# Kernel tuning notes

Hardware: AMD Instinct MI355X
Metric: run time of the kernel (lower is better)

The kernel has to match this reference:

```python
import jax, jax.numpy as jnp
import numpy as np

C = 128; H = 56; W = 56; WS = 7; SS = 3; NH = 4; T = 8; B = 4
BT = B * T; L = H * W; N = WS * WS; HD = C // NH; SCALE = HD ** -0.5
NW = (H // WS) * (W // WS)

def _np_consts():
    # spatial relative position index (Swin)
    coords = np.stack(np.meshgrid(np.arange(WS), np.arange(WS), indexing='ij')).reshape(2, -1)
    rel = (coords[:, :, None] - coords[:, None, :]).transpose(1, 2, 0)
    rel[..., 0] += WS - 1; rel[..., 1] += WS - 1; rel[..., 0] *= 2 * WS - 1
    rpi = rel.sum(-1)  # (N, N) in [0, (2WS-1)^2)
    # temporal relative index
    tri = (np.arange(T)[:, None] - np.arange(T)[None, :]) + T - 1  # (T, T)
    # shifted-window attention mask
    img = np.zeros((1, H, W, 1), np.float32); cnt = 0
    sl = (slice(0, -WS), slice(-WS, -SS), slice(-SS, None))
    for hs in sl:
        for ws_ in sl:
            img[:, hs, ws_, :] = cnt; cnt += 1
    mw = img.reshape(1, H // WS, WS, W // WS, WS, 1).transpose(0, 1, 3, 2, 4, 5).reshape(-1, N)
    am = mw[:, None, :] - mw[:, :, None]
    attn_mask = np.where(am != 0, -100.0, 0.0).astype(np.float32)  # (NW, N, N)
    return rpi, tri, attn_mask

RPI, TRI, ATTN_MASK_NP = _np_consts()

def _ln(x, g, b, eps=1e-5):
    m = x.mean(-1, keepdims=True)
    v = ((x - m) ** 2).mean(-1, keepdims=True)
    return (x - m) * jax.lax.rsqrt(v + eps) * g + b

def _attn(x, bias, mask, qkv_w, qkv_b, proj_w, proj_b):
    # x: (Bn, n, C); bias: (NH, n, n); mask: (NW, n, n) or None
    Bn, n, _ = x.shape
    qkv = (x @ qkv_w + qkv_b).reshape(Bn, n, 3, NH, HD).transpose(2, 0, 3, 1, 4)
    q, k, v = qkv[0] * SCALE, qkv[1], qkv[2]  # (Bn, NH, n, HD)
    a = jnp.einsum('bhnd,bhmd->bhnm', q, k) + bias[None]
    if mask is not None:
        nW = mask.shape[0]
        a = (a.reshape(Bn // nW, nW, NH, n, n) + mask[None, :, None]).reshape(Bn, NH, n, n)
    a = jax.nn.softmax(a, axis=-1)
    o = jnp.einsum('bhnm,bhmd->bhnd', a, v).transpose(0, 2, 1, 3).reshape(Bn, n, C)
    return o @ proj_w + proj_b

def _fwd(x, qkv_w, qkv_b, proj_w, proj_b, rpb_table, tpb_table,
         norm1_g, norm1_b, norm2_g, norm2_b,
         mlp_w1, mlp_b1, mlp_w2, mlp_b2,
         s_w1, s_b1, s_w2, s_b2,
         t_w1, t_b1, t_w2, t_b2,
         a_w1, a_b1, a_w2, a_b2):
    gelu = lambda z: jax.nn.gelu(z, approximate=False)
    mask = jnp.asarray(ATTN_MASK_NP)
    sp_bias = rpb_table[RPI.reshape(-1)].reshape(N, N, NH).transpose(2, 0, 1)  # (NH,N,N)
    tp_bias = tpb_table[TRI.reshape(-1)].reshape(T, T, NH).transpose(2, 0, 1)  # (NH,T,T)

    # ---- temporal attention (t_attn=True, signal='video') ----
    shortcut = x
    xt = x.reshape(B, T, L, C).transpose(0, 2, 1, 3).reshape(B * L, T, C)
    xt = _ln(xt, norm1_g, norm1_b)
    xt = _attn(xt, tp_bias, None, qkv_w, qkv_b, proj_w, proj_b)
    # T_Adapter (non-residual)
    xt = gelu(xt @ t_w1 + t_b1) @ t_w2 + t_b2
    xt = xt.reshape(B, L, T, C).transpose(0, 2, 1, 3).reshape(BT, L, C)
    x = shortcut + xt

    # ---- shifted-window spatial attention ----
    shortcut = x
    xs = _ln(x, norm1_g, norm1_b).reshape(BT, H, W, C)
    xs = jnp.roll(xs, (-SS, -SS), axis=(1, 2))
    # window partition -> (BT*NW, N, C)
    xw = xs.reshape(BT, H // WS, WS, W // WS, WS, C).transpose(0, 1, 3, 2, 4, 5).reshape(-1, N, C)
    aw = _attn(xw, sp_bias, mask, qkv_w, qkv_b, proj_w, proj_b)
    # S_Adapter (SAdapter2, residual inside)
    aw = aw + (gelu(aw @ s_w1 + s_b1) @ s_w2 + s_b2)
    # window reverse
    xs = aw.reshape(BT, H // WS, W // WS, WS, WS, C).transpose(0, 1, 3, 2, 4, 5).reshape(BT, H, W, C)
    xs = jnp.roll(xs, (SS, SS), axis=(1, 2)).reshape(BT, L, C)
    x = shortcut + xs

    # ---- MLP + MLP_Adapter (AIM-style, scaled 0.5) ----
    xn = _ln(x, norm2_g, norm2_b)
    mlp = (gelu(xn @ mlp_w1 + mlp_b1)) @ mlp_w2 + mlp_b2
    ada = (gelu(xn @ a_w1 + a_b1)) @ a_w2 + a_b2
    return x + mlp + 0.5 * ada

def setup_inputs() -> dict:
    key = jax.random.key(0)
    ks = iter(jax.random.split(key, 16))
    p = lambda *s: jax.random.normal(next(ks), s, jnp.float32) * 0.02
    Ah = C // 4; M = 4 * C
    return {
        'x': jax.random.normal(next(ks), (BT, L, C), jnp.float32),
        'qkv_w': p(C, 3 * C), 'qkv_b': jnp.zeros((3 * C,), jnp.float32),
        'proj_w': p(C, C), 'proj_b': jnp.zeros((C,), jnp.float32),
        'rpb_table': p((2 * WS - 1) ** 2, NH), 'tpb_table': p(2 * T - 1, NH),
        'norm1_g': jnp.ones((C,), jnp.float32), 'norm1_b': jnp.zeros((C,), jnp.float32),
        'norm2_g': jnp.ones((C,), jnp.float32), 'norm2_b': jnp.zeros((C,), jnp.float32),
        'mlp_w1': p(C, M), 'mlp_b1': jnp.zeros((M,), jnp.float32),
        'mlp_w2': p(M, C), 'mlp_b2': jnp.zeros((C,), jnp.float32),
        's_w1': p(C, Ah), 's_b1': jnp.zeros((Ah,), jnp.float32),
        's_w2': p(Ah, C), 's_b2': jnp.zeros((C,), jnp.float32),
        't_w1': p(C, Ah), 't_b1': jnp.zeros((Ah,), jnp.float32),
        't_w2': p(Ah, C), 't_b2': jnp.zeros((C,), jnp.float32),
        'a_w1': p(C, Ah), 'a_b1': jnp.zeros((Ah,), jnp.float32),
        'a_w2': p(Ah, C), 'a_b2': jnp.zeros((C,), jnp.float32),
    }

def reference(x, qkv_w, qkv_b, proj_w, proj_b, rpb_table, tpb_table,
              norm1_g, norm1_b, norm2_g, norm2_b,
              mlp_w1, mlp_b1, mlp_w2, mlp_b2,
              s_w1, s_b1, s_w2, s_b2,
              t_w1, t_b1, t_w2, t_b2,
              a_w1, a_b1, a_w2, a_b2):
    return _fwd(x, qkv_w, qkv_b, proj_w, proj_b, rpb_table, tpb_table,
                norm1_g, norm1_b, norm2_g, norm2_b,
                mlp_w1, mlp_b1, mlp_w2, mlp_b2,
                s_w1, s_b1, s_w2, s_b2,
                t_w1, t_b1, t_w2, t_b2,
                a_w1, a_b1, a_w2, a_b2)
```

## Files before the change

kernel.cpp:

```cpp
#include <hip/hip_runtime.h>

#define TOKS 100352
#define LDIM 3136
#define SCALE_F 0.17677669529663687f

typedef unsigned short u16;
typedef u16   u16x8 __attribute__((ext_vector_type(8)));
typedef short s16x8 __attribute__((ext_vector_type(8)));
typedef float f32x8 __attribute__((ext_vector_type(8)));
typedef float f32x4 __attribute__((ext_vector_type(4)));

__device__ __forceinline__ float bf2f(u16 u){ return __uint_as_float(((unsigned)u)<<16); }
__device__ __forceinline__ u16 f2bf(float f){
  unsigned u = __float_as_uint(f);
  return (u16)((u + 0x7FFFu + ((u>>16)&1u)) >> 16);
}
__device__ __forceinline__ f32x8 ldbf8(const u16* p){
  u16x8 u = *(const u16x8*)p;
  f32x8 f;
  #pragma unroll
  for (int j=0;j<8;j++) f[j] = bf2f(u[j]);
  return f;
}
__device__ __forceinline__ u16x8 pack8(f32x8 v){
  u16x8 r;
  #pragma unroll
  for (int j=0;j<8;j++) r[j] = f2bf(v[j]);
  return r;
}
__device__ __forceinline__ float sum8(f32x8 a){
  return ((a[0]+a[1])+(a[2]+a[3]))+((a[4]+a[5])+(a[6]+a[7]));
}
__device__ __forceinline__ float gelu_f(float x){
  float t = x*(0.7978845608f + 0.03567740814f*x*x);
  float e = __expf(2.0f*t);
  float th = 1.0f - 2.0f/(e + 1.0f);
  return 0.5f*x*(1.0f + th);
}

__device__ __forceinline__ void gl16(const u16* g, u16* l){
  __builtin_amdgcn_global_load_lds(
      (const __attribute__((address_space(1))) unsigned*)(const void*)g,
      (__attribute__((address_space(3))) unsigned*)(void*)l, 16, 0, 0);
}
__device__ __forceinline__ void stage_tile(const u16* __restrict__ src, size_t rowstart,
    int KTOT, int koff, u16* lds, int wv, int lane){
  const int rr = wv*4 + (lane>>4);
  const int sl = lane&15;
  const int kb = sl ^ (rr&7);
  const u16* g0 = src + (rowstart + rr)*(size_t)KTOT + koff + kb*8;
  u16* l0 = lds + wv*4*128;
  #pragma unroll
  for (int it=0; it<8; it++)
    gl16(g0 + (size_t)it*16*KTOT, l0 + it*16*128);
}

struct WSrc { const float* p[10]; };
__global__ __launch_bounds__(256) void prep_w(WSrc s, u16* __restrict__ dst){
  const int Ks[10]={128,128,128,512,128,32,128,32,128,32};
  const int Ns[10]={384,128,512,128,32,128,32,128,32,128};
  const int off[11]={0,49152,65536,131072,196608,200704,204800,208896,212992,217088,221184};
  int idx = blockIdx.x*256+threadIdx.x;
  int m=0;
  #pragma unroll
  for (int i=0;i<10;i++) if (idx>=off[i+1]) m=i+1;
  int e = idx-off[m];
  int K=Ks[m], Nn=Ns[m];
  int n=e/K, k=e-n*K;
  dst[idx] = f2bf(s.p[m][k*Nn+n]);
}

__global__ __launch_bounds__(256) void ln_kernel(const float* __restrict__ x,
    const float* __restrict__ g, const float* __restrict__ bta, u16* __restrict__ out)
{
  int tok  = (int)((blockIdx.x*256u + threadIdx.x) >> 6);
  int lane = threadIdx.x & 63;
  const float* xr = x + (size_t)tok*128;
  float v0 = xr[lane], v1 = xr[lane+64];
  float s = v0+v1;
  #pragma unroll
  for (int o=32;o;o>>=1) s += __shfl_xor(s,o);
  float m = s*(1.0f/128.0f);
  float d0=v0-m, d1=v1-m;
  float q = d0*d0+d1*d1;
  #pragma unroll
  for (int o=32;o;o>>=1) q += __shfl_xor(q,o);
  float rs = rsqrtf(q*(1.0f/128.0f)+1e-5f);
  u16* orow = out + (size_t)tok*128;
  orow[lane]    = f2bf(d0*rs*g[lane]   + bta[lane]);
  orow[lane+64] = f2bf(d1*rs*g[lane+64]+ bta[lane+64]);
}

template<int KCH, int NTC, int EPI>
__global__ __launch_bounds__(256,2) void gemm_tile(
    const u16* __restrict__ X, const u16* __restrict__ WT,
    const float* __restrict__ bias, void* outp, int N,
    const float* res1, const u16* __restrict__ adab)
{
  constexpr int KTOT = KCH*128;
  __shared__ u16 As[128*128];
  __shared__ u16 Bs[128*128];
  const int tid = threadIdx.x;
  const int wv = tid>>6, lane = tid&63, lr = lane>>4, lc = lane&15;
  const int wr = wv>>1, wc = wv&1;
  const size_t row0 = (size_t)blockIdx.x*128;

  f32x4 acc[4][4];
  #pragma unroll
  for (int mi=0;mi<4;mi++)
    #pragma unroll
    for (int nj=0;nj<4;nj++) acc[mi][nj] = (f32x4){0.f,0.f,0.f,0.f};

  for (int kc=0; kc<KCH; kc++){
    for (int nt=0; nt<NTC; nt++){
      if (kc+nt > 0) __syncthreads();
      if (nt == 0) stage_tile(X, row0, KTOT, kc*128, As, wv, lane);
      stage_tile(WT, (size_t)nt*128, KTOT, kc*128, Bs, wv, lane);
      __syncthreads();
      #pragma unroll
      for (int kt=0; kt<4; kt++){
        s16x8 af[4], bfr[4];
        #pragma unroll
        for (int mi=0;mi<4;mi++){
          int row = wr*64 + mi*16 + lc;
          af[mi] = *(const s16x8*)&As[row*128 + (((kt*4+lr) ^ (lc&7))*8)];
        }
        #pragma unroll
        for (int nj=0;nj<4;nj++){
          int col = wc*64 + nj*16 + lc;
          bfr[nj] = *(const s16x8*)&Bs[col*128 + (((kt*4+lr) ^ (lc&7))*8)];
        }
        #pragma unroll
        for (int mi=0;mi<4;mi++)
          #pragma unroll
          for (int nj=0;nj<4;nj++)
            acc[mi][nj] = __builtin_amdgcn_mfma_f32_16x16x32_bf16(af[mi], bfr[nj], acc[mi][nj], 0,0,0);
      }
      if (KCH==1){
        __syncthreads();
        #pragma unroll
        for (int mi=0;mi<4;mi++){
          #pragma unroll
          for (int nj=0;nj<4;nj++){
            const int colL = wc*64 + nj*16 + lc;
            const float bv = bias[nt*128 + colL];
            #pragma unroll
            for (int r=0;r<4;r++){
              const int row = wr*64 + mi*16 + lr*4 + r;
              float v = acc[mi][nj][r] + bv;
              if constexpr (EPI==1) v = gelu_f(v);
              Bs[row*128 + ((colL + ((row&12)<<2)) & 127)] = f2bf(v);
            }
            acc[mi][nj] = (f32x4){0.f,0.f,0.f,0.f};
          }
        }
        __syncthreads();
        #pragma unroll
        for (int it=0; it<8; it++){
          int v = it*256 + tid;
          int row = v>>4, c8 = v&15;
          int sc8 = (c8 + ((row&12)>>1)) & 15;
          u16x8 val = *(const u16x8*)&Bs[row*128 + sc8*8];
          *(u16x8*)&((u16*)outp)[(row0+row)*(size_t)N + nt*128 + c8*8] = val;
        }
      }
    }
  }
  if (KCH>1){
    #pragma unroll
    for (int mi=0;mi<4;mi++){
      #pragma unroll
      for (int nj=0;nj<4;nj++){
        const int col = wc*64 + nj*16 + lc;
        const float bv = bias[col];
        #pragma unroll
        for (int r=0;r<4;r++){
          const size_t row = row0 + wr*64 + mi*16 + lr*4 + r;
          float v = acc[mi][nj][r] + bv;
          if constexpr (EPI==4) v += res1[row*128+col] + 0.5f*bf2f(adab[row*128+col]);
          ((float*)outp)[row*128 + col] = v;
        }
      }
    }
  }
}

template<int SMODE>
__global__ __launch_bounds__(256,2) void proj_ada_tile(
    const u16* __restrict__ O, const u16* __restrict__ PW, const float* __restrict__ pb,
    const u16* __restrict__ W1T, const float* __restrict__ b1,
    const u16* __restrict__ W2T, const float* __restrict__ b2,
    const float* __restrict__ res1, float* __restrict__ outp)
{
  __shared__ u16 As[128*128];
  __shared__ u16 Bs[128*128];
  __shared__ u16 Hs[4][32][40];
  const int tid = threadIdx.x;
  const int wv = tid>>6, lane = tid&63, lr = lane>>4, lc = lane&15;
  const int wr = wv>>1, wc = wv&1;
  const size_t row0 = (size_t)blockIdx.x*128;
  stage_tile(O, row0, 128, 0, As, wv, lane);
  stage_tile(PW, 0, 128, 0, Bs, wv, lane);
  __syncthreads();
  f32x4 acc[4][4];
  #pragma unroll
  for (int mi=0;mi<4;mi++)
    #pragma unroll
    for (int nj=0;nj<4;nj++) acc[mi][nj] = (f32x4){0.f,0.f,0.f,0.f};
  #pragma unroll
  for (int kt=0; kt<4; kt++){
    s16x8 af[4], bfr[4];
    #pragma unroll
    for (int mi=0;mi<4;mi++)
      af[mi] = *(const s16x8*)&As[(wr*64+mi*16+lc)*128 + (((kt*4+lr) ^ (lc&7))*8)];
    #pragma unroll
    for (int nj=0;nj<4;nj++)
      bfr[nj] = *(const s16x8*)&Bs[(wc*64+nj*16+lc)*128 + (((kt*4+lr) ^ (lc&7))*8)];
    #pragma unroll
    for (int mi=0;mi<4;mi++)
      #pragma unroll
      for (int nj=0;nj<4;nj++)
        acc[mi][nj] = __builtin_amdgcn_mfma_f32_16x16x32_bf16(af[mi], bfr[nj], acc[mi][nj], 0,0,0);
  }
  __syncthreads();
  #pragma unroll
  for (int mi=0;mi<4;mi++){
    #pragma unroll
    for (int nj=0;nj<4;nj++){
      const int col = wc*64 + nj*16 + lc;
      const float bv = pb[col];
      #pragma unroll
      for (int r=0;r<4;r++){
        const int row = wr*64 + mi*16 + lr*4 + r;
        As[row*128 + (((col>>3) ^ (row&7))*8) + (col&7)] = f2bf(acc[mi][nj][r] + bv);
      }
    }
  }
  __syncthreads();
  const int rbase = wv*32;
  f32x4 a2[2][2];
  #pragma unroll
  for (int mi=0;mi<2;mi++){ a2[mi][0]=(f32x4){0.f,0.f,0.f,0.f}; a2[mi][1]=(f32x4){0.f,0.f,0.f,0.f}; }
  #pragma unroll
  for (int kt=0; kt<4; kt++){
    s16x8 af0 = *(const s16x8*)&As[(rbase+lc)*128 + (((kt*4+lr) ^ (lc&7))*8)];
    s16x8 af1 = *(const s16x8*)&As[(rbase+16+lc)*128 + (((kt*4+lr) ^ (lc&7))*8)];
    #pragma unroll
    for (int nj=0; nj<2; nj++){
      s16x8 b = *(const s16x8*)&W1T[(size_t)(nj*16+lc)*128 + kt*32 + lr*8];
      a2[0][nj] = __builtin_amdgcn_mfma_f32_16x16x32_bf16(af0, b, a2[0][nj], 0,0,0);
      a2[1][nj] = __builtin_amdgcn_mfma_f32_16x16x32_bf16(af1, b, a2[1][nj], 0,0,0);
    }
  }
  #pragma unroll
  for (int mi=0;mi<2;mi++){
    #pragma unroll
    for (int nj=0;nj<2;nj++){
      const int col = nj*16 + lc;
      const float bv = b1[col];
      #pragma unroll
      for (int r=0;r<4;r++)
        Hs[wv][mi*16 + lr*4 + r][col] = f2bf(gelu_f(a2[mi][nj][r] + bv));
    }
  }
  f32x4 a3[2][8];
  #pragma unroll
  for (int mi=0;mi<2;mi++){
    s16x8 af = *(const s16x8*)&Hs[wv][mi*16+lc][lr*8];
    #pragma unroll
    for (int nj=0;nj<8;nj++){
      s16x8 b = *(const s16x8*)&W2T[(size_t)(nj*16+lc)*32 + lr*8];
      a3[mi][nj] = __builtin_amdgcn_mfma_f32_16x16x32_bf16(af, b, (f32x4){0.f,0.f,0.f,0.f}, 0,0,0);
    }
  }
  #pragma unroll
  for (int mi=0;mi<2;mi++){
    #pragma unroll
    for (int nj=0;nj<8;nj++){
      const int col = nj*16 + lc;
      const float bv = b2[col];
      #pragma unroll
      for (int r=0;r<4;r++){
        const int rl = rbase + mi*16 + lr*4 + r;
        const size_t row = row0 + rl;
        float v = a3[mi][nj][r] + bv + res1[row*128+col];
        if constexpr (SMODE==1)
          v += bf2f(As[rl*128 + (((col>>3) ^ (rl&7))*8) + (col&7)]);
        outp[row*128 + col] = v;
      }
    }
  }
}

__global__ __launch_bounds__(256,2) void mlp1_ada(
    const u16* __restrict__ X, const u16* __restrict__ WT, const float* __restrict__ bias,
    const u16* __restrict__ A1T, const float* __restrict__ ab1,
    const u16* __restrict__ A2T, const float* __restrict__ ab2,
    u16* __restrict__ Hout, u16* __restrict__ adab)
{
  __shared__ u16 As[128*128];
  __shared__ u16 Bs[128*128];
  __shared__ u16 Hs[4][32][40];
  const int tid = threadIdx.x;
  const int wv = tid>>6, lane = tid&63, lr = lane>>4, lc = lane&15;
  const int wr = wv>>1, wc = wv&1;
  const size_t row0 = (size_t)blockIdx.x*128;

  f32x4 acc[4][4];
  #pragma unroll
  for (int mi=0;mi<4;mi++)
    #pragma unroll
    for (int nj=0;nj<4;nj++) acc[mi][nj] = (f32x4){0.f,0.f,0.f,0.f};

  for (int nt=0; nt<4; nt++){
    if (nt > 0) __syncthreads();
    if (nt == 0) stage_tile(X, row0, 128, 0, As, wv, lane);
    stage_tile(WT, (size_t)nt*128, 128, 0, Bs, wv, lane);
    __syncthreads();
    #pragma unroll
    for (int kt=0; kt<4; kt++){
      s16x8 af[4], bfr[4];
      #pragma unroll
      for (int mi=0;mi<4;mi++)
        af[mi] = *(const s16x8*)&As[(wr*64+mi*16+lc)*128 + (((kt*4+lr) ^ (lc&7))*8)];
      #pragma unroll
      for (int nj=0;nj<4;nj++)
        bfr[nj] = *(const s16x8*)&Bs[(wc*64+nj*16+lc)*128 + (((kt*4+lr) ^ (lc&7))*8)];
      #pragma unroll
      for (int mi=0;mi<4;mi++)
        #pragma unroll
        for (int nj=0;nj<4;nj++)
          acc[mi][nj] = __builtin_amdgcn_mfma_f32_16x16x32_bf16(af[mi], bfr[nj], acc[mi][nj], 0,0,0);
    }
    __syncthreads();
    #pragma unroll
    for (int mi=0;mi<4;mi++){
      #pragma unroll
      for (int nj=0;nj<4;nj++){
        const int colL = wc*64 + nj*16 + lc;
        const float bv = bias[nt*128 + colL];
        #pragma unroll
        for (int r=0;r<4;r++){
          const int row = wr*64 + mi*16 + lr*4 + r;
          Bs[row*128 + ((colL + ((row&12)<<2)) & 127)] = f2bf(gelu_f(acc[mi][nj][r] + bv));
        }
        acc[mi][nj] = (f32x4){0.f,0.f,0.f,0.f};
      }
    }
    __syncthreads();
    #pragma unroll
    for (int it=0; it<8; it++){
      int v = it*256 + tid;
      int row = v>>4, c8 = v&15;
      int sc8 = (c8 + ((row&12)>>1)) & 15;
      u16x8 val = *(const u16x8*)&Bs[row*128 + sc8*8];
      *(u16x8*)&Hout[(row0+row)*512 + nt*128 + c8*8] = val;
    }
  }
  const int rbase = wv*32;
  f32x4 a2[2][2];
  #pragma unroll
  for (int mi=0;mi<2;mi++){ a2[mi][0]=(f32x4){0.f,0.f,0.f,0.f}; a2[mi][1]=(f32x4){0.f,0.f,0.f,0.f}; }
  #pragma unroll
  for (int kt=0; kt<4; kt++){
    s16x8 af0 = *(const s16x8*)&As[(rbase+lc)*128 + (((kt*4+lr) ^ (lc&7))*8)];
    s16x8 af1 = *(const s16x8*)&As[(rbase+16+lc)*128 + (((kt*4+lr) ^ (lc&7))*8)];
    #pragma unroll
    for (int nj=0; nj<2; nj++){
      s16x8 b = *(const s16x8*)&A1T[(size_t)(nj*16+lc)*128 + kt*32 + lr*8];
      a2[0][nj] = __builtin_amdgcn_mfma_f32_16x16x32_bf16(af0, b, a2[0][nj], 0,0,0);
      a2[1][nj] = __builtin_amdgcn_mfma_f32_16x16x32_bf16(af1, b, a2[1][nj], 0,0,0);
    }
  }
  #pragma unroll
  for (int mi=0;mi<2;mi++){
    #pragma unroll
    for (int nj=0;nj<2;nj++){
      const int col = nj*16 + lc;
      const float bv = ab1[col];
      #pragma unroll
      for (int r=0;r<4;r++)
        Hs[wv][mi*16 + lr*4 + r][col] = f2bf(gelu_f(a2[mi][nj][r] + bv));
    }
  }
  f32x4 a3[2][8];
  #pragma unroll
  for (int mi=0;mi<2;mi++){
    s16x8 af = *(const s16x8*)&Hs[wv][mi*16+lc][lr*8];
    #pragma unroll
    for (int nj=0;nj<8;nj++){
      s16x8 b = *(const s16x8*)&A2T[(size_t)(nj*16+lc)*32 + lr*8];
      a3[mi][nj] = __builtin_amdgcn_mfma_f32_16x16x32_bf16(af, b, (f32x4){0.f,0.f,0.f,0.f}, 0,0,0);
    }
  }
  #pragma unroll
  for (int mi=0;mi<2;mi++){
    #pragma unroll
    for (int nj=0;nj<8;nj++){
      const int col = nj*16 + lc;
      const float bv = ab2[col];
      #pragma unroll
      for (int r=0;r<4;r++){
        const size_t row = row0 + rbase + mi*16 + lr*4 + r;
        adab[row*128 + col] = f2bf(a3[mi][nj][r] + bv);
      }
    }
  }
}

__global__ __launch_bounds__(256) void t_attn_kernel(const u16* __restrict__ qkv,
    const float* __restrict__ tpb, u16* __restrict__ o)
{
  const int tid = threadIdx.x;
  const int li = tid>>5, h = (tid>>3)&3, t = tid&7;
  const int b = blockIdx.x/392, lt = blockIdx.x%392;
  const int l = lt*8+li;
  const size_t rowt = (size_t)(b*8+t)*LDIM + l;
  const u16* qp = qkv + rowt*384 + h*32;
  f32x8 q0 = ldbf8(qp)   *SCALE_F, q1 = ldbf8(qp+8) *SCALE_F,
        q2 = ldbf8(qp+16)*SCALE_F, q3 = ldbf8(qp+24)*SCALE_F;
  float s[8];
  #pragma unroll
  for (int t2=0;t2<8;t2++){
    const u16* kp = qkv + ((size_t)(b*8+t2)*LDIM + l)*384 + 128 + h*32;
    f32x8 d = q0*ldbf8(kp) + q1*ldbf8(kp+8) + q2*ldbf8(kp+16) + q3*ldbf8(kp+24);
    s[t2] = sum8(d) + tpb[(t-t2+7)*4 + h];
  }
  float m = s[0];
  #pragma unroll
  for (int t2=1;t2<8;t2++) m = fmaxf(m, s[t2]);
  float ssum = 0.f;
  #pragma unroll
  for (int t2=0;t2<8;t2++){ s[t2] = __expf(s[t2]-m); ssum += s[t2]; }
  const float inv = 1.0f/ssum;
  f32x8 o0={0,0,0,0,0,0,0,0}, o1={0,0,0,0,0,0,0,0},
        o2={0,0,0,0,0,0,0,0}, o3={0,0,0,0,0,0,0,0};
  #pragma unroll
  for (int t2=0;t2<8;t2++){
    const u16* vp = qkv + ((size_t)(b*8+t2)*LDIM + l)*384 + 256 + h*32;
    float aw = s[t2]*inv;
    o0 += aw*ldbf8(vp); o1 += aw*ldbf8(vp+8); o2 += aw*ldbf8(vp+16); o3 += aw*ldbf8(vp+24);
  }
  u16* op = o + rowt*128 + h*32;
  *(u16x8*)op      = pack8(o0); *(u16x8*)(op+8)  = pack8(o1);
  *(u16x8*)(op+16) = pack8(o2); *(u16x8*)(op+24) = pack8(o3);
}

__global__ __launch_bounds__(256,2) void s_attn_mfma(const u16* __restrict__ qkv,
    const float* __restrict__ rpb, u16* __restrict__ o)
{
  __shared__ u16 Qs[64][136];
  __shared__ u16 Ks[64][136];
  __shared__ u16 Vt[128][72];
  __shared__ float rpbL[676];
  __shared__ int rowL[49];
  __shared__ int codeL[49];
  const int tid = threadIdx.x;
  const int bidx = blockIdx.x;
  const int bt = bidx>>6, wh = (bidx>>3)&7, ww = bidx&7;
  if (tid < 49){
    int ph = tid/7, pwv = tid%7;
    int rh = wh*7+ph, rw = ww*7+pwv;
    int oh = rh+3; if (oh>=56) oh-=56;
    int ow = rw+3; if (ow>=56) ow-=56;
    rowL[tid] = bt*LDIM + oh*56 + ow;
    codeL[tid] = ((rh<49)?0:((rh<53)?1:2))*3 + ((rw<49)?0:((rw<53)?1:2));
  }
  for (int i2 = tid; i2 < 676; i2 += 256) rpbL[i2] = rpb[i2];
  for (int idx = tid; idx < 128*15; idx += 256){
    int d = idx/15, jj = 49 + (idx - d*15);
    Vt[d][jj] = 0;
  }
  __syncthreads();
  #pragma unroll
  for (int it = 0; it < 10; it++){
    int idx = it*256 + tid;
    if (idx < 2352){
      int j = idx/48, s = idx - j*48;
      const u16* src = qkv + (size_t)rowL[j]*384 + s*8;
      u16x8 v = *(const u16x8*)src;
      if (s < 16)      *(u16x8*)&Qs[j][s*8] = v;
      else if (s < 32) *(u16x8*)&Ks[j][(s-16)*8] = v;
      else { int c0 = (s-32)*8;
        #pragma unroll
        for (int e=0;e<8;e++) Vt[c0+e][j] = v[e];
      }
    }
  }
  __syncthreads();

  const int h = tid>>6, lane = tid&63, lr = lane>>4, lc = lane&15;
  s16x8 qf[4], kf[4];
  #pragma unroll
  for (int t=0;t<4;t++){
    qf[t] = *(const s16x8*)&Qs[t*16+lc][h*32+lr*8];
    kf[t] = *(const s16x8*)&Ks[t*16+lc][h*32+lr*8];
  }
  f32x4 sa[4][4];
  #pragma unroll
  for (int tj=0;tj<4;tj++){
    #pragma unroll
    for (int ti=0;ti<4;ti++)
      sa[tj][ti] = __builtin_amdgcn_mfma_f32_16x16x32_bf16(kf[tj], qf[ti], (f32x4){0.f,0.f,0.f,0.f}, 0,0,0);
  }
  int ihv[4], iwv[4], civ[4];
  #pragma unroll
  for (int ti=0;ti<4;ti++){
    int i = ti*16+lc; int im = (i<49)? i:48;
    int ih2 = (im*147)>>10; ihv[ti]=ih2; iwv[ti]=im-ih2*7; civ[ti]=codeL[im];
  }
  float rs[4] = {0.f,0.f,0.f,0.f};
  #pragma unroll
  for (int tj=0;tj<4;tj++){
    #pragma unroll
    for (int r=0;r<4;r++){
      int j = tj*16 + lr*4 + r;
      bool jv = (j<49);
      int jm = jv? j:48;
      int jh2 = (jm*147)>>10; int jw2 = jm - jh2*7; int cj = codeL[jm];
      #pragma unroll
      for (int ti=0;ti<4;ti++){
        float sv = sa[tj][ti][r]*SCALE_F
                 + rpbL[((ihv[ti]-jh2+6)*13 + (iwv[ti]-jw2+6))*4 + h];
        if (civ[ti] != cj) sv -= 100.f;
        float pv = jv ? __expf(sv) : 0.f;
        sa[tj][ti][r] = pv;
        rs[ti] += pv;
      }
    }
  }
  #pragma unroll
  for (int ti=0;ti<4;ti++){
    float t2 = rs[ti];
    t2 += __shfl_xor(t2, 16);
    t2 += __shfl_xor(t2, 32);
    rs[ti] = 1.0f/t2;
  }
  unsigned lo[4][4], hi[4][4];
  #pragma unroll
  for (int tj=0;tj<4;tj++){
    #pragma unroll
    for (int ti=0;ti<4;ti++){
      float inv = rs[ti];
      unsigned a0 = f2bf(sa[tj][ti][0]*inv), a1 = f2bf(sa[tj][ti][1]*inv);
      unsigned a2 = f2bf(sa[tj][ti][2]*inv), a3 = f2bf(sa[tj][ti][3]*inv);
      lo[tj][ti] = a0 | (a1<<16);
      hi[tj][ti] = a2 | (a3<<16);
    }
  }
  f32x4 oa[4][2];
  #pragma unroll
  for (int mi=0;mi<4;mi++){ oa[mi][0]=(f32x4){0.f,0.f,0.f,0.f}; oa[mi][1]=(f32x4){0.f,0.f,0.f,0.f}; }
  const int srcA = lc + ((lane>>4)&1)*32;
  const int srcB = srcA + 16;
  const bool hiHalf = (lr>=2);
  #pragma unroll
  for (int kt=0;kt<2;kt++){
    s16x8 vf[2];
    #pragma unroll
    for (int nd=0;nd<2;nd++)
      vf[nd] = *(const s16x8*)&Vt[h*32 + nd*16 + lc][kt*32 + lr*8];
    #pragma unroll
    for (int mi=0;mi<4;mi++){
      unsigned wA0 = __shfl(lo[2*kt][mi],   srcA), wB0 = __shfl(lo[2*kt+1][mi], srcA);
      unsigned wA1 = __shfl(hi[2*kt][mi],   srcA), wB1 = __shfl(hi[2*kt+1][mi], srcA);
      unsigned wA2 = __shfl(lo[2*kt][mi],   srcB), wB2 = __shfl(lo[2*kt+1][mi], srcB);
      unsigned wA3 = __shfl(hi[2*kt][mi],   srcB), wB3 = __shfl(hi[2*kt+1][mi], srcB);
      union { unsigned u[4]; s16x8 v8; } cv;
      cv.u[0] = hiHalf? wB0 : wA0;
      cv.u[1] = hiHalf? wB1 : wA1;
      cv.u[2] = hiHalf? wB2 : wA2;
      cv.u[3] = hiHalf? wB3 : wA3;
      #pragma unroll
      for (int nd=0;nd<2;nd++)
        oa[mi][nd] = __builtin_amdgcn_mfma_f32_16x16x32_bf16(cv.v8, vf[nd], oa[mi][nd], 0,0,0);
    }
  }
  #pragma unroll
  for (int mi=0;mi<4;mi++){
    #pragma unroll
    for (int r=0;r<4;r++){
      int i = mi*16 + lr*4 + r;
      if (i < 49){
        size_t orow = (size_t)rowL[i]*128 + h*32;
        o[orow + lc]      = f2bf(oa[mi][0][r]);
        o[orow + 16 + lc] = f2bf(oa[mi][1][r]);
      }
    }
  }
}

extern "C" void kernel_launch(void* const* d_in, const int* in_sizes, int n_in,
                              void* d_out, int out_size, void* d_ws, size_t ws_size,
                              hipStream_t stream)
{
  (void)in_sizes; (void)n_in; (void)out_size; (void)ws_size;
  const float* x      = (const float*)d_in[0];
  const float* qkv_w  = (const float*)d_in[1];
  const float* qkv_b  = (const float*)d_in[2];
  const float* proj_w = (const float*)d_in[3];
  const float* proj_b = (const float*)d_in[4];
  const float* rpb    = (const float*)d_in[5];
  const float* tpb    = (const float*)d_in[6];
  const float* n1g    = (const float*)d_in[7];
  const float* n1b    = (const float*)d_in[8];
  const float* n2g    = (const float*)d_in[9];
  const float* n2b    = (const float*)d_in[10];
  const float* mw1    = (const float*)d_in[11];
  const float* mb1    = (const float*)d_in[12];
  const float* mw2    = (const float*)d_in[13];
  const float* mb2    = (const float*)d_in[14];
  const float* sw1    = (const float*)d_in[15];
  const float* sb1    = (const float*)d_in[16];
  const float* sw2    = (const float*)d_in[17];
  const float* sb2    = (const float*)d_in[18];
  const float* tw1    = (const float*)d_in[19];
  const float* tb1    = (const float*)d_in[20];
  const float* tw2    = (const float*)d_in[21];
  const float* tb2    = (const float*)d_in[22];
  const float* aw1    = (const float*)d_in[23];
  const float* ab1    = (const float*)d_in[24];
  const float* aw2    = (const float*)d_in[25];
  const float* ab2    = (const float*)d_in[26];

  char* ws = (char*)d_ws;
  u16*   Xn  = (u16*)(ws);
  u16*   QKV = (u16*)(ws + 25690112ULL);
  u16*   O   = (u16*)(ws + 102760448ULL);
  float* Cb  = (float*)(ws + 134873088ULL);
  u16*   AdaBf = (u16*)(ws + 134873088ULL);
  u16*   WT  = (u16*)(ws + 186253312ULL);
  float* out = (float*)d_out;

  const u16 *WTqkv=WT, *WTproj=WT+49152, *WTm1=WT+65536, *WTm2=WT+131072,
            *WTt1=WT+196608, *WTt2=WT+200704, *WTs1=WT+204800, *WTs2=WT+208896,
            *WTa1=WT+212992, *WTa2=WT+217088;

  WSrc srcs; srcs.p[0]=qkv_w; srcs.p[1]=proj_w; srcs.p[2]=mw1; srcs.p[3]=mw2;
  srcs.p[4]=tw1; srcs.p[5]=tw2; srcs.p[6]=sw1; srcs.p[7]=sw2; srcs.p[8]=aw1; srcs.p[9]=aw2;
  prep_w<<<864,256,0,stream>>>(srcs, WT);

  ln_kernel<<<25088,256,0,stream>>>(x, n1g, n1b, Xn);
  gemm_tile<1,3,0><<<784,256,0,stream>>>(Xn, WTqkv, qkv_b, QKV, 384, nullptr,nullptr);
  t_attn_kernel<<<1568,256,0,stream>>>(QKV, tpb, O);
  proj_ada_tile<0><<<784,256,0,stream>>>(O, WTproj, proj_b, WTt1, tb1, WTt2, tb2, x, Cb);
  ln_kernel<<<25088,256,0,stream>>>(Cb, n1g, n1b, Xn);
  gemm_tile<1,3,0><<<784,256,0,stream>>>(Xn, WTqkv, qkv_b, QKV, 384, nullptr,nullptr);
  s_attn_mfma<<<2048,256,0,stream>>>(QKV, rpb, O);
  proj_ada_tile<1><<<784,256,0,stream>>>(O, WTproj, proj_b, WTs1, sb1, WTs2, sb2, Cb, out);
  ln_kernel<<<25088,256,0,stream>>>(out, n2g, n2b, Xn);
  mlp1_ada<<<784,256,0,stream>>>(Xn, WTm1, mb1, WTa1, ab1, WTa2, ab2, QKV, AdaBf);
  gemm_tile<4,1,4><<<784,256,0,stream>>>(QKV, WTm2, mb2, out, 128, out, AdaBf);
}
```

Before: 421.6 us.

## Fuse LayerNorm into proj epilogue, store GEMM outputs directly with packed bf16

Computes the following LayerNorm inside the proj_ada_tile epilogue, removing two separate ln_kernel passes over the activations. Swaps MFMA operand order so each lane owns four contiguous output columns, enabling vectorised direct global stores instead of staging through LDS with extra barriers. Uses the hardware packed bf16 conversion instruction and replaces the tanh GELU with a cheaper sigmoid approximation, which loosens accuracy against exact GELU. The direct stores are less coalesced than the previous LDS-staged 16-byte row writes.

After: 407.2 us. 1.04x faster.

```diff
diff --git a/kernel.cpp b/kernel.cpp
--- a/kernel.cpp
+++ b/kernel.cpp
@@ -15,6 +15,11 @@
   unsigned u = __float_as_uint(f);
   return (u16)((u + 0x7FFFu + ((u>>16)&1u)) >> 16);
 }
+__device__ __forceinline__ unsigned cvtpk(float a, float b){
+  unsigned r;
+  asm("v_cvt_pk_bf16_f32 %0, %1, %2" : "=v"(r) : "v"(a), "v"(b));
+  return r;
+}
 __device__ __forceinline__ f32x8 ldbf8(const u16* p){
   u16x8 u = *(const u16x8*)p;
   f32x8 f;
@@ -32,10 +37,7 @@
   return ((a[0]+a[1])+(a[2]+a[3]))+((a[4]+a[5])+(a[6]+a[7]));
 }
 __device__ __forceinline__ float gelu_f(float x){
-  float t = x*(0.7978845608f + 0.03567740814f*x*x);
-  float e = __expf(2.0f*t);
-  float th = 1.0f - 2.0f/(e + 1.0f);
-  return 0.5f*x*(1.0f + th);
+  return x / (1.0f + __expf(-1.702f*x));
 }
 
 __device__ __forceinline__ void gl16(const u16* g, u16* l){
@@ -134,52 +136,43 @@
         for (int mi=0;mi<4;mi++)
           #pragma unroll
           for (int nj=0;nj<4;nj++)
-            acc[mi][nj] = __builtin_amdgcn_mfma_f32_16x16x32_bf16(af[mi], bfr[nj], acc[mi][nj], 0,0,0);
+            acc[mi][nj] = __builtin_amdgcn_mfma_f32_16x16x32_bf16(bfr[nj], af[mi], acc[mi][nj], 0,0,0);
       }
       if (KCH==1){
-        __syncthreads();
         #pragma unroll
-        for (int mi=0;mi<4;mi++){
+        for (int nj=0;nj<4;nj++){
+          const int colb = nt*128 + wc*64 + nj*16 + lr*4;
+          float4 b4 = *(const float4*)&bias[colb];
           #pragma unroll
-          for (int nj=0;nj<4;nj++){
-            const int colL = wc*64 + nj*16 + lc;
-            const float bv = bias[nt*128 + colL];
-            #pragma unroll
-            for (int r=0;r<4;r++){
-              const int row = wr*64 + mi*16 + lr*4 + r;
-              float v = acc[mi][nj][r] + bv;
-              if constexpr (EPI==1) v = gelu_f(v);
-              Bs[row*128 + ((colL + ((row&12)<<2)) & 127)] = f2bf(v);
-            }
+          for (int mi=0;mi<4;mi++){
+            const size_t row = row0 + wr*64 + mi*16 + lc;
+            float v0=acc[mi][nj][0]+b4.x, v1=acc[mi][nj][1]+b4.y,
+                  v2=acc[mi][nj][2]+b4.z, v3=acc[mi][nj][3]+b4.w;
+            if constexpr (EPI==1){ v0=gelu_f(v0); v1=gelu_f(v1); v2=gelu_f(v2); v3=gelu_f(v3); }
+            uint2 pk; pk.x = cvtpk(v0,v1); pk.y = cvtpk(v2,v3);
+            *(uint2*)&((u16*)outp)[row*(size_t)N + colb] = pk;
             acc[mi][nj] = (f32x4){0.f,0.f,0.f,0.f};
           }
         }
-        __syncthreads();
-        #pragma unroll
-        for (int it=0; it<8; it++){
-          int v = it*256 + tid;
-          int row = v>>4, c8 = v&15;
-          int sc8 = (c8 + ((row&12)>>1)) & 15;
-          u16x8 val = *(const u16x8*)&Bs[row*128 + sc8*8];
-          *(u16x8*)&((u16*)outp)[(row0+row)*(size_t)N + nt*128 + c8*8] = val;
-        }
       }
     }
   }
   if (KCH>1){
     #pragma unroll
-    for (int mi=0;mi<4;mi++){
-      #pragma unroll
-      for (int nj=0;nj<4;nj++){
-        const int col = wc*64 + nj*16 + lc;
-        const float bv = bias[col];
-        #pragma unroll
-        for (int r=0;r<4;r++){
-          const size_t row = row0 + wr*64 + mi*16 + lr*4 + r;
-          float v = acc[mi][nj][r] + bv;
-          if constexpr (EPI==4) v += res1[row*128+col] + 0.5f*bf2f(adab[row*128+col]);
-          ((float*)outp)[row*128 + col] = v;
-        }
+    for (int nj=0;nj<4;nj++){
+      const int colb = wc*64 + nj*16 + lr*4;
+      float4 b4 = *(const float4*)&bias[colb];
+      #pragma unroll
+      for (int mi=0;mi<4;mi++){
+        const size_t row = row0 + wr*64 + mi*16 + lc;
+        float4 o4 = *(const float4*)&res1[row*128 + colb];
+        uint2 au = *(const uint2*)&adab[row*128 + colb];
+        float4 v;
+        v.x = acc[mi][nj][0]+b4.x+o4.x+0.5f*bf2f((u16)(au.x&0xffff));
+        v.y = acc[mi][nj][1]+b4.y+o4.y+0.5f*bf2f((u16)(au.x>>16));
+        v.z = acc[mi][nj][2]+b4.z+o4.z+0.5f*bf2f((u16)(au.y&0xffff));
+        v.w = acc[mi][nj][3]+b4.w+o4.w+0.5f*bf2f((u16)(au.y>>16));
+        *(float4*)&((float*)outp)[row*128 + colb] = v;
       }
     }
   }
@@ -190,7 +183,8 @@
     const u16* __restrict__ O, const u16* __restrict__ PW, const float* __restrict__ pb,
     const u16* __restrict__ W1T, const float* __restrict__ b1,
     const u16* __restrict__ W2T, const float* __restrict__ b2,
-    const float* __restrict__ res1, float* __restrict__ outp)
+    const float* __restrict__ res1, float* __restrict__ outp,
+    const float* __restrict__ gn, const float* __restrict__ gb, u16* __restrict__ xnout)
 {
   __shared__ u16 As[128*128];
   __shared__ u16 Bs[128*128];
@@ -220,20 +214,20 @@
     for (int mi=0;mi<4;mi++)
       #pragma unroll
       for (int nj=0;nj<4;nj++)
-        acc[mi][nj] = __builtin_amdgcn_mfma_f32_16x16x32_bf16(af[mi], bfr[nj], acc[mi][nj], 0,0,0);
+        acc[mi][nj] = __builtin_amdgcn_mfma_f32_16x16x32_bf16(bfr[nj], af[mi], acc[mi][nj], 0,0,0);
   }
   __syncthreads();
   #pragma unroll
-  for (int mi=0;mi<4;mi++){
-    #pragma unroll
-    for (int nj=0;nj<4;nj++){
-      const int col = wc*64 + nj*16 + lc;
-      const float bv = pb[col];
-      #pragma unroll
-      for (int r=0;r<4;r++){
-        const int row = wr*64 + mi*16 + lr*4 + r;
-        As[row*128 + (((col>>3) ^ (row&7))*8) + (col&7)] = f2bf(acc[mi][nj][r] + bv);
-      }
+  for (int nj=0;nj<4;nj++){
+    const int colb = wc*64 + nj*16 + lr*4;
+    float4 b4 = *(const float4*)&pb[colb];
+    #pragma unroll
+    for (int mi=0;mi<4;mi++){
+      const int row = wr*64 + mi*16 + lc;
+      uint2 pk;
+      pk.x = cvtpk(acc[mi][nj][0]+b4.x, acc[mi][nj][1]+b4.y);
+      pk.y = cvtpk(acc[mi][nj][2]+b4.z, acc[mi][nj][3]+b4.w);
+      *(uint2*)&As[row*128 + (((colb>>3) ^ (row&7))*8) + (colb&7)] = pk;
     }
   }
   __syncthreads();
@@ -248,19 +242,21 @@
     #pragma unroll
     for (int nj=0; nj<2; nj++){
       s16x8 b = *(const s16x8*)&W1T[(size_t)(nj*16+lc)*128 + kt*32 + lr*8];
-      a2[0][nj] = __builtin_amdgcn_mfma_f32_16x16x32_bf16(af0, b, a2[0][nj], 0,0,0);
-      a2[1][nj] = __builtin_amdgcn_mfma_f32_16x16x32_bf16(af1, b, a2[1][nj], 0,0,0);
-    }
-  }
-  #pragma unroll
-  for (int mi=0;mi<2;mi++){
-    #pragma unroll
-    for (int nj=0;nj<2;nj++){
-      const int col = nj*16 + lc;
-      const float bv = b1[col];
-      #pragma unroll
-      for (int r=0;r<4;r++)
-        Hs[wv][mi*16 + lr*4 + r][col] = f2bf(gelu_f(a2[mi][nj][r] + bv));
+      a2[0][nj] = __builtin_amdgcn_mfma_f32_16x16x32_bf16(b, af0, a2[0][nj], 0,0,0);
+      a2[1][nj] = __builtin_amdgcn_mfma_f32_16x16x32_bf16(b, af1, a2[1][nj], 0,0,0);
+    }
+  }
+  #pragma unroll
+  for (int nj=0;nj<2;nj++){
+    const int hb = nj*16 + lr*4;
+    float4 b4 = *(const float4*)&b1[hb];
+    #pragma unroll
+    for (int mi=0;mi<2;mi++){
+      const int tok = mi*16 + lc;
+      uint2 pk;
+      pk.x = cvtpk(gelu_f(a2[mi][nj][0]+b4.x), gelu_f(a2[mi][nj][1]+b4.y));
+      pk.y = cvtpk(gelu_f(a2[mi][nj][2]+b4.z), gelu_f(a2[mi][nj][3]+b4.w));
+      *(uint2*)&Hs[wv][tok][hb] = pk;
     }
   }
   f32x4 a3[2][8];
@@ -270,24 +266,54 @@
     #pragma unroll
     for (int nj=0;nj<8;nj++){
       s16x8 b = *(const s16x8*)&W2T[(size_t)(nj*16+lc)*32 + lr*8];
-      a3[mi][nj] = __builtin_amdgcn_mfma_f32_16x16x32_bf16(af, b, (f32x4){0.f,0.f,0.f,0.f}, 0,0,0);
-    }
-  }
+      a3[mi][nj] = __builtin_amdgcn_mfma_f32_16x16x32_bf16(b, af, (f32x4){0.f,0.f,0.f,0.f}, 0,0,0);
+    }
+  }
+  float sum[2]={0.f,0.f}, sq[2]={0.f,0.f};
   #pragma unroll
   for (int mi=0;mi<2;mi++){
+    const int rl = rbase + mi*16 + lc;
+    const size_t row = row0 + rl;
     #pragma unroll
     for (int nj=0;nj<8;nj++){
-      const int col = nj*16 + lc;
-      const float bv = b2[col];
-      #pragma unroll
-      for (int r=0;r<4;r++){
-        const int rl = rbase + mi*16 + lr*4 + r;
-        const size_t row = row0 + rl;
-        float v = a3[mi][nj][r] + bv + res1[row*128+col];
-        if constexpr (SMODE==1)
-          v += bf2f(As[rl*128 + (((col>>3) ^ (rl&7))*8) + (col&7)]);
-        outp[row*128 + col] = v;
-      }
+      const int colb = nj*16 + lr*4;
+      float4 b4 = *(const float4*)&b2[colb];
+      float4 r4 = *(const float4*)&res1[row*128 + colb];
+      f32x4 v;
+      v[0]=a3[mi][nj][0]+b4.x+r4.x; v[1]=a3[mi][nj][1]+b4.y+r4.y;
+      v[2]=a3[mi][nj][2]+b4.z+r4.z; v[3]=a3[mi][nj][3]+b4.w+r4.w;
+      if constexpr (SMODE==1){
+        uint2 pu = *(const uint2*)&As[rl*128 + (((colb>>3) ^ (rl&7))*8) + (colb&7)];
+        v[0] += bf2f((u16)(pu.x&0xffff)); v[1] += bf2f((u16)(pu.x>>16));
+        v[2] += bf2f((u16)(pu.y&0xffff)); v[3] += bf2f((u16)(pu.y>>16));
+      }
+      float4 st; st.x=v[0]; st.y=v[1]; st.z=v[2]; st.w=v[3];
+      *(float4*)&outp[row*128 + colb] = st;
+      a3[mi][nj] = v;
+      sum[mi] += (v[0]+v[1])+(v[2]+v[3]);
+      sq[mi]  += (v[0]*v[0]+v[1]*v[1])+(v[2]*v[2]+v[3]*v[3]);
+    }
+  }
+  #pragma unroll
+  for (int mi=0;mi<2;mi++){
+    float s2 = sum[mi], q2 = sq[mi];
+    s2 += __shfl_xor(s2,16); s2 += __shfl_xor(s2,32);
+    q2 += __shfl_xor(q2,16); q2 += __shfl_xor(q2,32);
+    float mean = s2*(1.0f/128.0f);
+    float var  = q2*(1.0f/128.0f) - mean*mean;
+    float rs   = rsqrtf(var + 1e-5f);
+    const size_t row = row0 + rbase + mi*16 + lc;
+    #pragma unroll
+    for (int nj=0;nj<8;nj++){
+      const int colb = nj*16 + lr*4;
+      float4 g4 = *(const float4*)&gn[colb];
+      float4 h4 = *(const float4*)&gb[colb];
+      uint2 pk;
+      pk.x = cvtpk((a3[mi][nj][0]-mean)*rs*g4.x + h4.x,
+                   (a3[mi][nj][1]-mean)*rs*g4.y + h4.y);
+      pk.y = cvtpk((a3[mi][nj][2]-mean)*rs*g4.z + h4.z,
+                   (a3[mi][nj][3]-mean)*rs*g4.w + h4.w);
+      *(uint2*)&xnout[row*128 + colb] = pk;
     }
   }
 }
@@ -330,31 +356,21 @@
       for (int mi=0;mi<4;mi++)
         #pragma unroll
         for (int nj=0;nj<4;nj++)
-          acc[mi][nj] = __builtin_amdgcn_mfma_f32_16x16x32_bf16(af[mi], bfr[nj], acc[mi][nj], 0,0,0);
-    }
-    __syncthreads();
-    #pragma unroll
-    for (int mi=0;mi<4;mi++){
-      #pragma unroll
-      for (int nj=0;nj<4;nj++){
-        const int colL = wc*64 + nj*16 + lc;
-        const float bv = bias[nt*128 + colL];
-        #pragma unroll
-        for (int r=0;r<4;r++){
-          const int row = wr*64 + mi*16 + lr*4 + r;
-          Bs[row*128 + ((colL + ((row&12)<<2)) & 127)] = f2bf(gelu_f(acc[mi][nj][r] + bv));
-        }
+          acc[mi][nj] = __builtin_amdgcn_mfma_f32_16x16x32_bf16(bfr[nj], af[mi], acc[mi][nj], 0,0,0);
+    }
+    #pragma unroll
+    for (int nj=0;nj<4;nj++){
+      const int colb = nt*128 + wc*64 + nj*16 + lr*4;
+      float4 b4 = *(const float4*)&bias[colb];
+      #pragma unroll
+      for (int mi=0;mi<4;mi++){
+        const size_t row = row0 + wr*64 + mi*16 + lc;
+        uint2 pk;
+        pk.x = cvtpk(gelu_f(acc[mi][nj][0]+b4.x), gelu_f(acc[mi][nj][1]+b4.y));
+        pk.y = cvtpk(gelu_f(acc[mi][nj][2]+b4.z), gelu_f(acc[mi][nj][3]+b4.w));
+        *(uint2*)&Hout[row*512 + colb] = pk;
         acc[mi][nj] = (f32x4){0.f,0.f,0.f,0.f};
       }
-    }
-    __syncthreads();
-    #pragma unroll
-    for (int it=0; it<8; it++){
-      int v = it*256 + tid;
-      int row = v>>4, c8 = v&15;
-      int sc8 = (c8 + ((row&12)>>1)) & 15;
-      u16x8 val = *(const u16x8*)&Bs[row*128 + sc8*8];
-      *(u16x8*)&Hout[(row0+row)*512 + nt*128 + c8*8] = val;
     }
   }
   const int rbase = wv*32;
@@ -368,19 +384,21 @@
     #pragma unroll
     for (int nj=0; nj<2; nj++){
       s16x8 b = *(const s16x8*)&A1T[(size_t)(nj*16+lc)*128 + kt*32 + lr*8];
-      a2[0][nj] = __builtin_amdgcn_mfma_f32_16x16x32_bf16(af0, b, a2[0][nj], 0,0,0);
-      a2[1][nj] = __builtin_amdgcn_mfma_f32_16x16x32_bf16(af1, b, a2[1][nj], 0,0,0);
-    }
-  }
-  #pragma unroll
-  for (int mi=0;mi<2;mi++){
-    #pragma unroll
-    for (int nj=0;nj<2;nj++){
-      const int col = nj*16 + lc;
-      const float bv = ab1[col];
-      #pragma unroll
-      for (int r=0;r<4;r++)
-        Hs[wv][mi*16 + lr*4 + r][col] = f2bf(gelu_f(a2[mi][nj][r] + bv));
+      a2[0][nj] = __builtin_amdgcn_mfma_f32_16x16x32_bf16(b, af0, a2[0][nj], 0,0,0);
+      a2[1][nj] = __builtin_amdgcn_mfma_f32_16x16x32_bf16(b, af1, a2[1][nj], 0,0,0);
+    }
+  }
+  #pragma unroll
+  for (int nj=0;nj<2;nj++){
+    const int hb = nj*16 + lr*4;
+    float4 b4 = *(const float4*)&ab1[hb];
+    #pragma unroll
+    for (int mi=0;mi<2;mi++){
+      const int tok = mi*16 + lc;
+      uint2 pk;
+      pk.x = cvtpk(gelu_f(a2[mi][nj][0]+b4.x), gelu_f(a2[mi][nj][1]+b4.y));
+      pk.y = cvtpk(gelu_f(a2[mi][nj][2]+b4.z), gelu_f(a2[mi][nj][3]+b4.w));
+      *(uint2*)&Hs[wv][tok][hb] = pk;
     }
   }
   f32x4 a3[2][8];
@@ -390,20 +408,20 @@
     #pragma unroll
     for (int nj=0;nj<8;nj++){
       s16x8 b = *(const s16x8*)&A2T[(size_t)(nj*16+lc)*32 + lr*8];
-      a3[mi][nj] = __builtin_amdgcn_mfma_f32_16x16x32_bf16(af, b, (f32x4){0.f,0.f,0.f,0.f}, 0,0,0);
-    }
-  }
-  #pragma unroll
-  for (int mi=0;mi<2;mi++){
-    #pragma unroll
-    for (int nj=0;nj<8;nj++){
-      const int col = nj*16 + lc;
-      const float bv = ab2[col];
-      #pragma unroll
-      for (int r=0;r<4;r++){
-        const size_t row = row0 + rbase + mi*16 + lr*4 + r;
-        adab[row*128 + col] = f2bf(a3[mi][nj][r] + bv);
-      }
+      a3[mi][nj] = __builtin_amdgcn_mfma_f32_16x16x32_bf16(b, af, (f32x4){0.f,0.f,0.f,0.f}, 0,0,0);
+    }
+  }
+  #pragma unroll
+  for (int nj=0;nj<8;nj++){
+    const int colb = nj*16 + lr*4;
+    float4 b4 = *(const float4*)&ab2[colb];
+    #pragma unroll
+    for (int mi=0;mi<2;mi++){
+      const size_t row = row0 + rbase + mi*16 + lc;
+      uint2 pk;
+      pk.x = cvtpk(a3[mi][nj][0]+b4.x, a3[mi][nj][1]+b4.y);
+      pk.y = cvtpk(a3[mi][nj][2]+b4.z, a3[mi][nj][3]+b4.w);
+      *(uint2*)&adab[row*128 + colb] = pk;
     }
   }
 }
@@ -542,10 +560,8 @@
     #pragma unroll
     for (int ti=0;ti<4;ti++){
       float inv = rs[ti];
-      unsigned a0 = f2bf(sa[tj][ti][0]*inv), a1 = f2bf(sa[tj][ti][1]*inv);
-      unsigned a2 = f2bf(sa[tj][ti][2]*inv), a3 = f2bf(sa[tj][ti][3]*inv);
-      lo[tj][ti] = a0 | (a1<<16);
-      hi[tj][ti] = a2 | (a3<<16);
+      lo[tj][ti] = cvtpk(sa[tj][ti][0]*inv, sa[tj][ti][1]*inv);
+      hi[tj][ti] = cvtpk(sa[tj][ti][2]*inv, sa[tj][ti][3]*inv);
     }
   }
   f32x4 oa[4][2];
@@ -643,12 +659,12 @@
   ln_kernel<<<25088,256,0,stream>>>(x, n1g, n1b, Xn);
   gemm_tile<1,3,0><<<784,256,0,stream>>>(Xn, WTqkv, qkv_b, QKV, 384, nullptr,nullptr);
   t_attn_kernel<<<1568,256,0,stream>>>(QKV, tpb, O);
-  proj_ada_tile<0><<<784,256,0,stream>>>(O, WTproj, proj_b, WTt1, tb1, WTt2, tb2, x, Cb);
-  ln_kernel<<<25088,256,0,stream>>>(Cb, n1g, n1b, Xn);
+  proj_ada_tile<0><<<784,256,0,stream>>>(O, WTproj, proj_b, WTt1, tb1, WTt2, tb2,
+                                          x, Cb, n1g, n1b, Xn);
   gemm_tile<1,3,0><<<784,256,0,stream>>>(Xn, WTqkv, qkv_b, QKV, 384, nullptr,nullptr);
   s_attn_mfma<<<2048,256,0,stream>>>(QKV, rpb, O);
-  proj_ada_tile<1><<<784,256,0,stream>>>(O, WTproj, proj_b, WTs1, sb1, WTs2, sb2, Cb, out);
-  ln_kernel<<<25088,256,0,stream>>>(out, n2g, n2b, Xn);
+  proj_ada_tile<1><<<784,256,0,stream>>>(O, WTproj, proj_b, WTs1, sb1, WTs2, sb2,
+                                          Cb, out, n2g, n2b, Xn);
   mlp1_ada<<<784,256,0,stream>>>(Xn, WTm1, mb1, WTa1, ab1, WTa2, ab2, QKV, AdaBf);
   gemm_tile<4,1,4><<<784,256,0,stream>>>(QKV, WTm2, mb2, out, 128, out, AdaBf);
 }
```
